# Kernel optimization log

Measured on AMD Instinct MI355X. Metric: run time of the kernel, lower is better.

Reference implementation:

```python
import jax, jax.numpy as jnp
import numpy as np

B, N = 8, 2048
IN_DIM, MEM_DIM, CTX_DIM = 256, 256, 128

def _linear_params(key, out_dim, in_dim):
    kw, kb = jax.random.split(key)
    bound = 1.0 / np.sqrt(in_dim)
    W = jax.random.uniform(kw, (out_dim, in_dim), jnp.float32, -bound, bound)
    b = jax.random.uniform(kb, (out_dim,), jnp.float32, -bound, bound)
    return W, b

def setup_inputs() -> dict:
    key = jax.random.key(0)
    ks = jax.random.split(key, 8)
    Wq, bq = _linear_params(ks[0], CTX_DIM, IN_DIM)
    Wk, bk = _linear_params(ks[1], CTX_DIM, MEM_DIM)
    Wv, bv = _linear_params(ks[2], MEM_DIM, MEM_DIM)
    Wu, bu = _linear_params(ks[3], MEM_DIM, IN_DIM + MEM_DIM)
    Wr, br = _linear_params(ks[4], MEM_DIM, IN_DIM + MEM_DIM)
    Wc, bc = _linear_params(ks[5], MEM_DIM, IN_DIM + MEM_DIM)
    input_tensor = jax.random.normal(ks[6], (B, N, IN_DIM), jnp.float32)
    previous_memory = jax.random.normal(ks[7], (B, N, MEM_DIM), jnp.float32)
    return dict(input_tensor=input_tensor, previous_memory=previous_memory,
                Wq=Wq, bq=bq, Wk=Wk, bk=bk, Wv=Wv, bv=bv,
                Wu=Wu, bu=bu, Wr=Wr, br=br, Wc=Wc, bc=bc)

def reference(input_tensor, previous_memory, Wq, bq, Wk, bk, Wv, bv, Wu, bu, Wr, br, Wc, bc):
    # QKV projections (torch Linear: y = x @ W.T + b)
    query = jnp.einsum('bnd,cd->bnc', input_tensor, Wq) + bq        # [B,N,CTX]
    key = jnp.einsum('bnm,cm->bnc', previous_memory, Wk) + bk       # [B,N,CTX]
    value = jnp.einsum('bnm,vm->bnv', previous_memory, Wv) + bv     # [B,N,MEM]
    attention_scores = jnp.einsum('bqc,bkc->bqk', query, key)        # [B,N,N]
    attention_probs = jax.nn.softmax(attention_scores, axis=-1)
    context_vector = jnp.einsum('bqk,bkv->bqv', attention_probs, value)  # computed but unused downstream, as in original
    combined = jnp.concatenate([input_tensor, previous_memory], axis=-1)  # [B,N,IN+MEM]
    update_gate = jax.nn.sigmoid(jnp.einsum('bnd,md->bnm', combined, Wu) + bu)
    reset_gate = jax.nn.sigmoid(jnp.einsum('bnd,md->bnm', combined, Wr) + br)
    cand_in = jnp.concatenate([input_tensor, reset_gate * previous_memory], axis=-1)
    candidate_memory = jnp.tanh(jnp.einsum('bnd,md->bnm', cand_in, Wc) + bc)
    new_memory = (1.0 - update_gate) * previous_memory + update_gate * candidate_memory
    return new_memory, attention_probs
```

## Files before the change

kernel.cpp:

```cpp
#include <hip/hip_runtime.h>


typedef _Float16 half8 __attribute__((ext_vector_type(8)));
typedef _Float16 half4 __attribute__((ext_vector_type(4)));
typedef float floatx4 __attribute__((ext_vector_type(4)));

#define MFMA16(a, b, c) __builtin_amdgcn_mfma_f32_16x16x32_f16((a), (b), (c), 0, 0, 0)

#define OFF_WQH 0
#define OFF_WQL 32768
#define OFF_WKH 65536
#define OFF_WKL 98304
#define OFF_WUH 131072
#define OFF_WRH 262144
#define OFF_WCH 393216
#define OFF_Q   524288
#define OFF_K   2621440

__device__ __forceinline__ void gload16(const void* g, void* l) {
  __builtin_amdgcn_global_load_lds((const __attribute__((address_space(1))) unsigned int*)g,
                                   (__attribute__((address_space(3))) unsigned int*)l, 16, 0, 0);
}

__global__ __launch_bounds__(256) void k0_convert(
    const float* __restrict__ Wq, const float* __restrict__ Wk,
    const float* __restrict__ Wu, const float* __restrict__ Wr,
    const float* __restrict__ Wc, _Float16* __restrict__ ws)
{
  int i = blockIdx.x * 256 + threadIdx.x;
  if (i < 32768) {
    float w = Wq[i];
    _Float16 h = (_Float16)w;
    ws[OFF_WQH + i] = h;
    ws[OFF_WQL + i] = (_Float16)(w - (float)h);
  } else if (i < 65536) {
    int j = i - 32768;
    float w = Wk[j];
    _Float16 h = (_Float16)w;
    ws[OFF_WKH + j] = h;
    ws[OFF_WKL + j] = (_Float16)(w - (float)h);
  } else {
    int j = i - 65536;
    if (j < 131072)      ws[OFF_WUH + j]            = (_Float16)Wu[j];
    else if (j < 262144) ws[OFF_WRH + (j - 131072)] = (_Float16)Wr[j - 131072];
    else                 ws[OFF_WCH + (j - 262144)] = (_Float16)Wc[j - 262144];
  }
}

__global__ __launch_bounds__(512) void k1_proj(
    const float* __restrict__ input, const float* __restrict__ prev,
    const float* __restrict__ bq, const float* __restrict__ bk,
    _Float16* __restrict__ ws)
{
  __shared__ char smem[2 * 8192];
  const int which = blockIdx.y;
  const float* x = which ? prev : input;
  const _Float16* WH = ws + (which ? OFF_WKH : OFF_WQH);
  const _Float16* WL = ws + (which ? OFF_WKL : OFF_WQL);
  const float* bias = which ? bk : bq;
  _Float16* out = ws + (which ? OFF_K : OFF_Q);

  const int tid = threadIdx.x, w = tid >> 6, l = tid & 63;
  const int lr = l & 15, lg = l >> 4;
  const int rows0 = blockIdx.x * 64;
  const int c = w * 16 + lr;

  half8 bh[8], blo[8];
#pragma unroll
  for (int ks = 0; ks < 8; ++ks) {
    bh[ks]  = *(const half8*)(WH + (size_t)c * 256 + ks * 32 + lg * 8);
    blo[ks] = *(const half8*)(WL + (size_t)c * 256 + ks * 32 + lg * 8);
  }
  const float bv = bias[c];

  const int srow = tid >> 5, scol = (tid & 31) * 8;
  const int ssz = (srow & 7) << 4;
  floatx4 st0, st1;

#define K1_LOAD(ch) { const float* src = x + ((size_t)rows0 + (ch) * 16 + srow) * 256 + scol; \
  st0 = *(const floatx4*)src; st1 = *(const floatx4*)(src + 4); }
#define K1_WRITE(ch) { char* bufw = smem + ((ch) & 1) * 8192; \
  half8 h; \
  _Pragma("unroll") for (int j = 0; j < 4; ++j) { \
    h[j] = (_Float16)st0[j]; h[4+j] = (_Float16)st1[j]; } \
  *(half8*)(bufw + srow * 512 + ((scol * 2) ^ ssz)) = h; }

  K1_LOAD(0); K1_WRITE(0);
  __syncthreads();
#pragma unroll 1
  for (int ch = 0; ch < 4; ++ch) {
    if (ch < 3) K1_LOAD(ch + 1);
    const char* buf = smem + (ch & 1) * 8192;
    floatx4 acc = {0.f, 0.f, 0.f, 0.f};
    const int base = lr * 512, sz = (lr & 7) << 4;
#pragma unroll
    for (int ks = 0; ks < 8; ++ks) {
      half8 ah = *(const half8*)(buf + base + ((ks * 64 + lg * 16) ^ sz));
      acc = MFMA16(ah, bh[ks], acc);
      acc = MFMA16(ah, blo[ks], acc);
    }
#pragma unroll
    for (int j = 0; j < 4; ++j)
      out[((size_t)rows0 + ch * 16 + lg * 4 + j) * 128 + c] = (_Float16)(acc[j] + bv);
    if (ch < 3) K1_WRITE(ch + 1);
    __syncthreads();
  }
}

__global__ __launch_bounds__(512) void k2ru(
    const float* __restrict__ input, const float* __restrict__ prev,
    const float* __restrict__ br, const float* __restrict__ bu,
    const _Float16* __restrict__ ws,
    _Float16* __restrict__ t_sc, _Float16* __restrict__ u_sc)
{
  __shared__ char smem[2 * 16384];
  const int tid = threadIdx.x, w = tid >> 6, l = tid & 63;
  const int lr = l & 15, lg = l >> 4;
  const int rows0 = blockIdx.x * 128;
  const int isU = w >> 2;
  const int c = blockIdx.y * 64 + (w & 3) * 16 + lr;

  const _Float16* W = ws + (isU ? OFF_WUH : OFF_WRH);
  half8 bw[16];
#pragma unroll
  for (int ks = 0; ks < 16; ++ks)
    bw[ks] = *(const half8*)(W + (size_t)c * 512 + ks * 32 + lg * 8);
  const float bv = (isU ? bu : br)[c];

  const int srow = tid >> 5, scol = (tid & 31) * 8;
  const int ssz = (srow & 7) << 4;
  floatx4 sI0, sI1, sP0, sP1;

#define K2RU_LOAD(ch) { \
  const float* si = input + ((size_t)rows0 + (ch) * 16 + srow) * 256 + scol; \
  const float* sp = prev  + ((size_t)rows0 + (ch) * 16 + srow) * 256 + scol; \
  sI0 = *(const floatx4*)si; sI1 = *(const floatx4*)(si + 4); \
  sP0 = *(const floatx4*)sp; sP1 = *(const floatx4*)(sp + 4); }
#define K2RU_WRITE(ch) { char* bufw = smem + ((ch) & 1) * 16384; \
  half8 hi, hp; \
  _Pragma("unroll") for (int j = 0; j < 4; ++j) { \
    hi[j] = (_Float16)sI0[j]; hi[4+j] = (_Float16)sI1[j]; \
    hp[j] = (_Float16)sP0[j]; hp[4+j] = (_Float16)sP1[j]; } \
  int o = srow * 1024 + ((scol * 2) ^ ssz); \
  *(half8*)(bufw + o) = hi; *(half8*)(bufw + o + 512) = hp; }

  K2RU_LOAD(0); K2RU_WRITE(0);
  __syncthreads();
#pragma unroll 1
  for (int ch = 0; ch < 8; ++ch) {
    if (ch < 7) K2RU_LOAD(ch + 1);
    const char* buf = smem + (ch & 1) * 16384;
    floatx4 acc = {0.f, 0.f, 0.f, 0.f};
    const int base = lr * 1024, sz = (lr & 7) << 4;
#pragma unroll
    for (int ks = 0; ks < 16; ++ks) {
      half8 a = *(const half8*)(buf + base + ((ks * 64 + lg * 16) ^ sz));
      acc = MFMA16(a, bw[ks], acc);
    }
#pragma unroll
    for (int j = 0; j < 4; ++j) {
      const int crow = lg * 4 + j;
      const size_t grow = (size_t)rows0 + ch * 16 + crow;
      float g = 1.f / (1.f + __expf(-(acc[j] + bv)));
      if (!isU) {
        float m = (float)*(const _Float16*)(buf + crow * 1024 + 512 + ((c * 2) ^ ((crow & 7) << 4)));
        t_sc[grow * 256 + c] = (_Float16)(g * m);
      } else {
        u_sc[grow * 256 + c] = (_Float16)g;
      }
    }
    if (ch < 7) K2RU_WRITE(ch + 1);
    __syncthreads();
  }
}

__global__ __launch_bounds__(512) void k2c(
    const float* __restrict__ input, const float* __restrict__ prev,
    const float* __restrict__ bc, const _Float16* __restrict__ ws,
    const _Float16* __restrict__ t_sc, const _Float16* __restrict__ u_sc,
    float* __restrict__ out0)
{
  __shared__ char smem[2 * 16384];
  const int tid = threadIdx.x, w = tid >> 6, l = tid & 63;
  const int lr = l & 15, lg = l >> 4;
  const int rows0 = blockIdx.x * 64;
  const int c = blockIdx.y * 128 + w * 16 + lr;

  half8 bw[16];
#pragma unroll
  for (int ks = 0; ks < 16; ++ks)
    bw[ks] = *(const half8*)(ws + OFF_WCH + (size_t)c * 512 + ks * 32 + lg * 8);
  const float bv = bc[c];

  const int srow = tid >> 5, scol = (tid & 31) * 8;
  const int ssz = (srow & 7) << 4;
  floatx4 sI0, sI1;
  half8 sT;

#define K2C_LOAD(ch) { \
  const float* si = input + ((size_t)rows0 + (ch) * 16 + srow) * 256 + scol; \
  sI0 = *(const floatx4*)si; sI1 = *(const floatx4*)(si + 4); \
  sT = *(const half8*)(t_sc + ((size_t)rows0 + (ch) * 16 + srow) * 256 + scol); }
#define K2C_WRITE(ch) { char* bufw = smem + ((ch) & 1) * 16384; \
  half8 hi; \
  _Pragma("unroll") for (int j = 0; j < 4; ++j) { hi[j] = (_Float16)sI0[j]; hi[4+j] = (_Float16)sI1[j]; } \
  int o = srow * 1024 + ((scol * 2) ^ ssz); \
  *(half8*)(bufw + o) = hi; *(half8*)(bufw + o + 512) = sT; }

  K2C_LOAD(0); K2C_WRITE(0);
  __syncthreads();
#pragma unroll 1
  for (int ch = 0; ch < 4; ++ch) {
    if (ch < 3) K2C_LOAD(ch + 1);
    const char* buf = smem + (ch & 1) * 16384;
    floatx4 acc = {0.f, 0.f, 0.f, 0.f};
    const int base = lr * 1024, sz = (lr & 7) << 4;
#pragma unroll
    for (int ks = 0; ks < 16; ++ks) {
      half8 a = *(const half8*)(buf + base + ((ks * 64 + lg * 16) ^ sz));
      acc = MFMA16(a, bw[ks], acc);
    }
#pragma unroll
    for (int j = 0; j < 4; ++j) {
      const size_t grow = (size_t)rows0 + ch * 16 + lg * 4 + j;
      float e2 = __expf(2.f * (acc[j] + bv));
      float cg = (e2 - 1.f) / (e2 + 1.f);
      float u = (float)u_sc[grow * 256 + c];
      float m = prev[grow * 256 + c];
      out0[grow * 256 + c] = (1.f - u) * m + u * cg;
    }
    if (ch < 3) K2C_WRITE(ch + 1);
    __syncthreads();
  }
}

#define K3_STAGE(Kg, dst, ch) { \
  const char* g_ = (Kg) + (ch) * 32768; \
  _Pragma("unroll") for (int i_ = 0; i_ < 4; ++i_) { \
    int o_ = w * 1024 + i_ * 8192 + l * 16; \
    int row_ = o_ >> 8, col_ = o_ & 255; \
    gload16(g_ + row_ * 256 + (col_ ^ ((row_ & 7) << 4)), (dst) + w * 1024 + i_ * 8192); } }

__global__ __launch_bounds__(512) void k3a_sums(
    const _Float16* __restrict__ ws, float* __restrict__ part)
{
  __shared__ char kbuf[2][32768];
  const int b = blockIdx.x, q0 = blockIdx.y * 128, kh = blockIdx.z;
  const int tid = threadIdx.x, w = tid >> 6, l = tid & 63;
  const int lr = l & 15, lg = l >> 4;

  const _Float16* Q = ws + OFF_Q + ((size_t)b * 2048 + q0 + w * 16) * 128;
  const char* Kg = (const char*)(ws + OFF_K + ((size_t)b * 2048 + kh * 512) * 128);

  half8 qf[4];
#pragma unroll
  for (int ks = 0; ks < 4; ++ks)
    qf[ks] = *(const half8*)(Q + (size_t)lr * 128 + ks * 32 + lg * 8);

  K3_STAGE(Kg, kbuf[0], 0);
  __syncthreads();

  float se = 0.f;
#pragma unroll 1
  for (int ch = 0; ch < 4; ++ch) {
    if (ch < 3) K3_STAGE(Kg, kbuf[(ch + 1) & 1], ch + 1);
    const char* buf = kbuf[ch & 1];
#pragma unroll
    for (int kt = 0; kt < 8; ++kt) {
      const int kk = kt * 16 + lr;
      const int kbase = kk * 256, ksz = (kk & 7) << 4;
      half8 kf[4];
#pragma unroll
      for (int ks = 0; ks < 4; ++ks)
        kf[ks] = *(const half8*)(buf + kbase + ((ks * 64 + lg * 16) ^ ksz));
      floatx4 acc = {0.f, 0.f, 0.f, 0.f};
#pragma unroll
      for (int ks = 0; ks < 4; ++ks) acc = MFMA16(kf[ks], qf[ks], acc);
#pragma unroll
      for (int j = 0; j < 4; ++j) se += __expf(acc[j] - 14.f);
    }
    __syncthreads();
  }
  se += __shfl_xor(se, 16);
  se += __shfl_xor(se, 32);
  if (lg == 0)
    part[((size_t)b * 4 + kh) * 2048 + q0 + w * 16 + lr] = se;
}

__global__ __launch_bounds__(512) void k3b_store(
    const _Float16* __restrict__ ws, const float* __restrict__ part,
    float* __restrict__ out1)
{
  __shared__ char kbuf[2][32768];
  const int b = blockIdx.x, q0 = blockIdx.y * 128, kh = blockIdx.z;
  const int tid = threadIdx.x, w = tid >> 6, l = tid & 63;
  const int lr = l & 15, lg = l >> 4;

  const int q = q0 + w * 16 + lr;
  const _Float16* Q = ws + OFF_Q + ((size_t)b * 2048 + q0 + w * 16) * 128;
  const char* Kg = (const char*)(ws + OFF_K + ((size_t)b * 2048 + kh * 512) * 128);

  half8 qf[4];
#pragma unroll
  for (int ks = 0; ks < 4; ++ks)
    qf[ks] = *(const half8*)(Q + (size_t)lr * 128 + ks * 32 + lg * 8);
  const float inv = 1.f / (part[(size_t)(b * 4 + 0) * 2048 + q] +
                           part[(size_t)(b * 4 + 1) * 2048 + q] +
                           part[(size_t)(b * 4 + 2) * 2048 + q] +
                           part[(size_t)(b * 4 + 3) * 2048 + q]);

  K3_STAGE(Kg, kbuf[0], 0);
  __syncthreads();

  float* orow = out1 + ((size_t)b * 2048 + q) * 2048 + kh * 512;
#pragma unroll 1
  for (int ch = 0; ch < 4; ++ch) {
    if (ch < 3) K3_STAGE(Kg, kbuf[(ch + 1) & 1], ch + 1);
    const char* buf = kbuf[ch & 1];
#pragma unroll
    for (int kt = 0; kt < 8; ++kt) {
      const int kk = kt * 16 + lr;
      const int kbase = kk * 256, ksz = (kk & 7) << 4;
      half8 kf[4];
#pragma unroll
      for (int ks = 0; ks < 4; ++ks)
        kf[ks] = *(const half8*)(buf + kbase + ((ks * 64 + lg * 16) ^ ksz));
      floatx4 acc = {0.f, 0.f, 0.f, 0.f};
#pragma unroll
      for (int ks = 0; ks < 4; ++ks) acc = MFMA16(kf[ks], qf[ks], acc);
      floatx4 v;
#pragma unroll
      for (int j = 0; j < 4; ++j) v[j] = __expf(acc[j] - 14.f) * inv;
      *(floatx4*)(orow + ch * 128 + kt * 16 + lg * 4) = v;
    }
    __syncthreads();
  }
}

extern "C" void kernel_launch(void* const* d_in, const int* in_sizes, int n_in,
                              void* d_out, int out_size, void* d_ws, size_t ws_size,
                              hipStream_t stream)
{
  const float* input = (const float*)d_in[0];
  const float* prev  = (const float*)d_in[1];
  const float* Wq = (const float*)d_in[2];
  const float* bq = (const float*)d_in[3];
  const float* Wk = (const float*)d_in[4];
  const float* bk = (const float*)d_in[5];
  const float* Wu = (const float*)d_in[8];
  const float* bu = (const float*)d_in[9];
  const float* Wr = (const float*)d_in[10];
  const float* br = (const float*)d_in[11];
  const float* Wc = (const float*)d_in[12];
  const float* bc = (const float*)d_in[13];

  float* out0 = (float*)d_out;
  float* out1 = out0 + (size_t)8 * 2048 * 256;
  _Float16* ws = (_Float16*)d_ws;

  _Float16* t_sc = (_Float16*)out1;
  _Float16* u_sc = (_Float16*)out1 + 4194304;
  float* part = (float*)ws;

  hipLaunchKernelGGL(k0_convert, dim3(1792), dim3(256), 0, stream, Wq, Wk, Wu, Wr, Wc, ws);
  hipLaunchKernelGGL(k1_proj,    dim3(256, 2), dim3(512), 0, stream, input, prev, bq, bk, ws);
  hipLaunchKernelGGL(k2ru,       dim3(128, 4), dim3(512), 0, stream, input, prev, br, bu, ws, t_sc, u_sc);
  hipLaunchKernelGGL(k2c,        dim3(256, 2), dim3(512), 0, stream, input, prev, bc, ws, t_sc, u_sc, out0);
  hipLaunchKernelGGL(k3a_sums,   dim3(8, 16, 4), dim3(512), 0, stream, ws, part);
  hipLaunchKernelGGL(k3b_store,  dim3(8, 16, 4), dim3(512), 0, stream, ws, part, out1);
}
```

Measured before the change: 109.5 us.

## Merge independent stages into two fused launches and convert weights inline

```diff
diff --git a/kernel.cpp b/kernel.cpp
--- a/kernel.cpp
+++ b/kernel.cpp
@@ -7,13 +7,6 @@
 
 #define MFMA16(a, b, c) __builtin_amdgcn_mfma_f32_16x16x32_f16((a), (b), (c), 0, 0, 0)
 
-#define OFF_WQH 0
-#define OFF_WQL 32768
-#define OFF_WKH 65536
-#define OFF_WKL 98304
-#define OFF_WUH 131072
-#define OFF_WRH 262144
-#define OFF_WCH 393216
 #define OFF_Q   524288
 #define OFF_K   2621440
 
@@ -22,114 +15,41 @@
                                    (__attribute__((address_space(3))) unsigned int*)l, 16, 0, 0);
 }
 
-__global__ __launch_bounds__(256) void k0_convert(
-    const float* __restrict__ Wq, const float* __restrict__ Wk,
-    const float* __restrict__ Wu, const float* __restrict__ Wr,
-    const float* __restrict__ Wc, _Float16* __restrict__ ws)
+__global__ __launch_bounds__(512, 4) void kA(
+    const float* __restrict__ input, const float* __restrict__ prev,
+    const float* __restrict__ Wq, const float* __restrict__ bq,
+    const float* __restrict__ Wk, const float* __restrict__ bk,
+    const float* __restrict__ Wr, const float* __restrict__ br,
+    const float* __restrict__ Wu, const float* __restrict__ bu,
+    _Float16* __restrict__ ws,
+    _Float16* __restrict__ t_sc, _Float16* __restrict__ u_sc)
 {
-  int i = blockIdx.x * 256 + threadIdx.x;
-  if (i < 32768) {
-    float w = Wq[i];
-    _Float16 h = (_Float16)w;
-    ws[OFF_WQH + i] = h;
-    ws[OFF_WQL + i] = (_Float16)(w - (float)h);
-  } else if (i < 65536) {
-    int j = i - 32768;
-    float w = Wk[j];
-    _Float16 h = (_Float16)w;
-    ws[OFF_WKH + j] = h;
-    ws[OFF_WKL + j] = (_Float16)(w - (float)h);
-  } else {
-    int j = i - 65536;
-    if (j < 131072)      ws[OFF_WUH + j]            = (_Float16)Wu[j];
-    else if (j < 262144) ws[OFF_WRH + (j - 131072)] = (_Float16)Wr[j - 131072];
-    else                 ws[OFF_WCH + (j - 262144)] = (_Float16)Wc[j - 262144];
-  }
-}
-
-__global__ __launch_bounds__(512) void k1_proj(
-    const float* __restrict__ input, const float* __restrict__ prev,
-    const float* __restrict__ bq, const float* __restrict__ bk,
-    _Float16* __restrict__ ws)
-{
-  __shared__ char smem[2 * 8192];
-  const int which = blockIdx.y;
-  const float* x = which ? prev : input;
-  const _Float16* WH = ws + (which ? OFF_WKH : OFF_WQH);
-  const _Float16* WL = ws + (which ? OFF_WKL : OFF_WQL);
-  const float* bias = which ? bk : bq;
-  _Float16* out = ws + (which ? OFF_K : OFF_Q);
-
+  __shared__ char smem[32768];
   const int tid = threadIdx.x, w = tid >> 6, l = tid & 63;
   const int lr = l & 15, lg = l >> 4;
-  const int rows0 = blockIdx.x * 64;
-  const int c = w * 16 + lr;
-
-  half8 bh[8], blo[8];
-#pragma unroll
-  for (int ks = 0; ks < 8; ++ks) {
-    bh[ks]  = *(const half8*)(WH + (size_t)c * 256 + ks * 32 + lg * 8);
-    blo[ks] = *(const half8*)(WL + (size_t)c * 256 + ks * 32 + lg * 8);
-  }
-  const float bv = bias[c];
-
-  const int srow = tid >> 5, scol = (tid & 31) * 8;
-  const int ssz = (srow & 7) << 4;
-  floatx4 st0, st1;
-
-#define K1_LOAD(ch) { const float* src = x + ((size_t)rows0 + (ch) * 16 + srow) * 256 + scol; \
-  st0 = *(const floatx4*)src; st1 = *(const floatx4*)(src + 4); }
-#define K1_WRITE(ch) { char* bufw = smem + ((ch) & 1) * 8192; \
-  half8 h; \
-  _Pragma("unroll") for (int j = 0; j < 4; ++j) { \
-    h[j] = (_Float16)st0[j]; h[4+j] = (_Float16)st1[j]; } \
-  *(half8*)(bufw + srow * 512 + ((scol * 2) ^ ssz)) = h; }
-
-  K1_LOAD(0); K1_WRITE(0);
-  __syncthreads();
-#pragma unroll 1
-  for (int ch = 0; ch < 4; ++ch) {
-    if (ch < 3) K1_LOAD(ch + 1);
-    const char* buf = smem + (ch & 1) * 8192;
-    floatx4 acc = {0.f, 0.f, 0.f, 0.f};
-    const int base = lr * 512, sz = (lr & 7) << 4;
-#pragma unroll
-    for (int ks = 0; ks < 8; ++ks) {
-      half8 ah = *(const half8*)(buf + base + ((ks * 64 + lg * 16) ^ sz));
-      acc = MFMA16(ah, bh[ks], acc);
-      acc = MFMA16(ah, blo[ks], acc);
-    }
-#pragma unroll
-    for (int j = 0; j < 4; ++j)
-      out[((size_t)rows0 + ch * 16 + lg * 4 + j) * 128 + c] = (_Float16)(acc[j] + bv);
-    if (ch < 3) K1_WRITE(ch + 1);
-    __syncthreads();
-  }
-}
-
-__global__ __launch_bounds__(512) void k2ru(
-    const float* __restrict__ input, const float* __restrict__ prev,
-    const float* __restrict__ br, const float* __restrict__ bu,
-    const _Float16* __restrict__ ws,
-    _Float16* __restrict__ t_sc, _Float16* __restrict__ u_sc)
-{
-  __shared__ char smem[2 * 16384];
-  const int tid = threadIdx.x, w = tid >> 6, l = tid & 63;
-  const int lr = l & 15, lg = l >> 4;
-  const int rows0 = blockIdx.x * 128;
-  const int isU = w >> 2;
-  const int c = blockIdx.y * 64 + (w & 3) * 16 + lr;
-
-  const _Float16* W = ws + (isU ? OFF_WUH : OFF_WRH);
-  half8 bw[16];
-#pragma unroll
-  for (int ks = 0; ks < 16; ++ks)
-    bw[ks] = *(const half8*)(W + (size_t)c * 512 + ks * 32 + lg * 8);
-  const float bv = (isU ? bu : br)[c];
-
-  const int srow = tid >> 5, scol = (tid & 31) * 8;
-  const int ssz = (srow & 7) << 4;
-  floatx4 sI0, sI1, sP0, sP1;
+
+  if (blockIdx.x < 512) {
+    const int b2 = blockIdx.x;
+    const int rows0 = (b2 & 127) * 128;
+    const int isU = w >> 2;
+    const int c = (b2 >> 7) * 64 + (w & 3) * 16 + lr;
+
+    const float* Wf = isU ? Wu : Wr;
+    half8 bw[16];
+#pragma unroll
+    for (int ks = 0; ks < 16; ++ks) {
+      floatx4 w0 = *(const floatx4*)(Wf + (size_t)c * 512 + ks * 32 + lg * 8);
+      floatx4 w1 = *(const floatx4*)(Wf + (size_t)c * 512 + ks * 32 + lg * 8 + 4);
+      half8 h;
+#pragma unroll
+      for (int j = 0; j < 4; ++j) { h[j] = (_Float16)w0[j]; h[4 + j] = (_Float16)w1[j]; }
+      bw[ks] = h;
+    }
+    const float bv = (isU ? bu : br)[c];
+
+    const int srow = tid >> 5, scol = (tid & 31) * 8;
+    const int ssz = (srow & 7) << 4;
+    floatx4 sI0, sI1, sP0, sP1;
 
 #define K2RU_LOAD(ch) { \
   const float* si = input + ((size_t)rows0 + (ch) * 16 + srow) * 256 + scol; \
@@ -144,58 +64,176 @@
   int o = srow * 1024 + ((scol * 2) ^ ssz); \
   *(half8*)(bufw + o) = hi; *(half8*)(bufw + o + 512) = hp; }
 
-  K2RU_LOAD(0); K2RU_WRITE(0);
-  __syncthreads();
-#pragma unroll 1
-  for (int ch = 0; ch < 8; ++ch) {
-    if (ch < 7) K2RU_LOAD(ch + 1);
-    const char* buf = smem + (ch & 1) * 16384;
-    floatx4 acc = {0.f, 0.f, 0.f, 0.f};
-    const int base = lr * 1024, sz = (lr & 7) << 4;
-#pragma unroll
-    for (int ks = 0; ks < 16; ++ks) {
-      half8 a = *(const half8*)(buf + base + ((ks * 64 + lg * 16) ^ sz));
-      acc = MFMA16(a, bw[ks], acc);
-    }
-#pragma unroll
-    for (int j = 0; j < 4; ++j) {
-      const int crow = lg * 4 + j;
-      const size_t grow = (size_t)rows0 + ch * 16 + crow;
-      float g = 1.f / (1.f + __expf(-(acc[j] + bv)));
-      if (!isU) {
-        float m = (float)*(const _Float16*)(buf + crow * 1024 + 512 + ((c * 2) ^ ((crow & 7) << 4)));
-        t_sc[grow * 256 + c] = (_Float16)(g * m);
-      } else {
-        u_sc[grow * 256 + c] = (_Float16)g;
-      }
-    }
-    if (ch < 7) K2RU_WRITE(ch + 1);
-    __syncthreads();
+    K2RU_LOAD(0); K2RU_WRITE(0);
+    __syncthreads();
+#pragma unroll 1
+    for (int ch = 0; ch < 8; ++ch) {
+      if (ch < 7) K2RU_LOAD(ch + 1);
+      const char* buf = smem + (ch & 1) * 16384;
+      floatx4 acc = {0.f, 0.f, 0.f, 0.f};
+      const int base = lr * 1024, sz = (lr & 7) << 4;
+#pragma unroll
+      for (int ks = 0; ks < 16; ++ks) {
+        half8 a = *(const half8*)(buf + base + ((ks * 64 + lg * 16) ^ sz));
+        acc = MFMA16(a, bw[ks], acc);
+      }
+#pragma unroll
+      for (int j = 0; j < 4; ++j) {
+        const int crow = lg * 4 + j;
+        const size_t grow = (size_t)rows0 + ch * 16 + crow;
+        float g = 1.f / (1.f + __expf(-(acc[j] + bv)));
+        if (!isU) {
+          float m = (float)*(const _Float16*)(buf + crow * 1024 + 512 + ((c * 2) ^ ((crow & 7) << 4)));
+          t_sc[grow * 256 + c] = (_Float16)(g * m);
+        } else {
+          u_sc[grow * 256 + c] = (_Float16)g;
+        }
+      }
+      if (ch < 7) K2RU_WRITE(ch + 1);
+      __syncthreads();
+    }
+  } else {
+    const int b1 = blockIdx.x - 512;
+    const int which = b1 >> 8;
+    const int rows0 = (b1 & 255) * 64;
+    const float* x = which ? prev : input;
+    const float* Wf = which ? Wk : Wq;
+    const float* bias = which ? bk : bq;
+    _Float16* out = ws + (which ? OFF_K : OFF_Q);
+    const int c = w * 16 + lr;
+
+    half8 bh[8], blo[8];
+#pragma unroll
+    for (int ks = 0; ks < 8; ++ks) {
+      floatx4 w0 = *(const floatx4*)(Wf + (size_t)c * 256 + ks * 32 + lg * 8);
+      floatx4 w1 = *(const floatx4*)(Wf + (size_t)c * 256 + ks * 32 + lg * 8 + 4);
+      half8 h, lo;
+#pragma unroll
+      for (int j = 0; j < 4; ++j) {
+        _Float16 h0 = (_Float16)w0[j];
+        h[j] = h0; lo[j] = (_Float16)(w0[j] - (float)h0);
+        _Float16 h1 = (_Float16)w1[j];
+        h[4 + j] = h1; lo[4 + j] = (_Float16)(w1[j] - (float)h1);
+      }
+      bh[ks] = h; blo[ks] = lo;
+    }
+    const float bv = bias[c];
+
+    const int srow = tid >> 5, scol = (tid & 31) * 8;
+    const int ssz = (srow & 7) << 4;
+    floatx4 st0, st1;
+
+#define K1_LOAD(ch) { const float* src = x + ((size_t)rows0 + (ch) * 16 + srow) * 256 + scol; \
+  st0 = *(const floatx4*)src; st1 = *(const floatx4*)(src + 4); }
+#define K1_WRITE(ch) { char* bufw = smem + ((ch) & 1) * 8192; \
+  half8 h; \
+  _Pragma("unroll") for (int j = 0; j < 4; ++j) { \
+    h[j] = (_Float16)st0[j]; h[4+j] = (_Float16)st1[j]; } \
+  *(half8*)(bufw + srow * 512 + ((scol * 2) ^ ssz)) = h; }
+
+    K1_LOAD(0); K1_WRITE(0);
+    __syncthreads();
+#pragma unroll 1
+    for (int ch = 0; ch < 4; ++ch) {
+      if (ch < 3) K1_LOAD(ch + 1);
+      const char* buf = smem + (ch & 1) * 8192;
+      floatx4 acc = {0.f, 0.f, 0.f, 0.f};
+      const int base = lr * 512, sz = (lr & 7) << 4;
+#pragma unroll
+      for (int ks = 0; ks < 8; ++ks) {
+        half8 ah = *(const half8*)(buf + base + ((ks * 64 + lg * 16) ^ sz));
+        acc = MFMA16(ah, bh[ks], acc);
+        acc = MFMA16(ah, blo[ks], acc);
+      }
+#pragma unroll
+      for (int j = 0; j < 4; ++j)
+        out[((size_t)rows0 + ch * 16 + lg * 4 + j) * 128 + c] = (_Float16)(acc[j] + bv);
+      if (ch < 3) K1_WRITE(ch + 1);
+      __syncthreads();
+    }
   }
 }
 
-__global__ __launch_bounds__(512) void k2c(
+#define K3_STAGE(Kg, dst, ch) { \
+  const char* g_ = (Kg) + (ch) * 32768; \
+  _Pragma("unroll") for (int i_ = 0; i_ < 4; ++i_) { \
+    int o_ = w * 1024 + i_ * 8192 + l * 16; \
+    int row_ = o_ >> 8, col_ = o_ & 255; \
+    gload16(g_ + row_ * 256 + (col_ ^ ((row_ & 7) << 4)), (dst) + w * 1024 + i_ * 8192); } }
+
+__global__ __launch_bounds__(512, 4) void kB(
     const float* __restrict__ input, const float* __restrict__ prev,
-    const float* __restrict__ bc, const _Float16* __restrict__ ws,
+    const float* __restrict__ Wc, const float* __restrict__ bc,
+    const _Float16* __restrict__ ws, float* __restrict__ part,
     const _Float16* __restrict__ t_sc, const _Float16* __restrict__ u_sc,
     float* __restrict__ out0)
 {
-  __shared__ char smem[2 * 16384];
+  __shared__ char smem[65536];
   const int tid = threadIdx.x, w = tid >> 6, l = tid & 63;
   const int lr = l & 15, lg = l >> 4;
-  const int rows0 = blockIdx.x * 64;
-  const int c = blockIdx.y * 128 + w * 16 + lr;
-
-  half8 bw[16];
-#pragma unroll
-  for (int ks = 0; ks < 16; ++ks)
-    bw[ks] = *(const half8*)(ws + OFF_WCH + (size_t)c * 512 + ks * 32 + lg * 8);
-  const float bv = bc[c];
-
-  const int srow = tid >> 5, scol = (tid & 31) * 8;
-  const int ssz = (srow & 7) << 4;
-  floatx4 sI0, sI1;
-  half8 sT;
+
+  if (blockIdx.x < 512) {
+    const int b3 = blockIdx.x;
+    const int b = b3 & 7, q0 = ((b3 >> 3) & 15) * 128, kh = b3 >> 7;
+
+    const _Float16* Q = ws + OFF_Q + ((size_t)b * 2048 + q0 + w * 16) * 128;
+    const char* Kg = (const char*)(ws + OFF_K + ((size_t)b * 2048 + kh * 512) * 128);
+
+    half8 qf[4];
+#pragma unroll
+    for (int ks = 0; ks < 4; ++ks)
+      qf[ks] = *(const half8*)(Q + (size_t)lr * 128 + ks * 32 + lg * 8);
+
+    char* kbuf0 = smem, * kbuf1 = smem + 32768;
+    K3_STAGE(Kg, kbuf0, 0);
+    __syncthreads();
+
+    float se = 0.f;
+#pragma unroll 1
+    for (int ch = 0; ch < 4; ++ch) {
+      if (ch < 3) K3_STAGE(Kg, ((ch + 1) & 1) ? kbuf1 : kbuf0, ch + 1);
+      const char* buf = (ch & 1) ? kbuf1 : kbuf0;
+#pragma unroll
+      for (int kt = 0; kt < 8; ++kt) {
+        const int kk = kt * 16 + lr;
+        const int kbase = kk * 256, ksz = (kk & 7) << 4;
+        half8 kf[4];
+#pragma unroll
+        for (int ks = 0; ks < 4; ++ks)
+          kf[ks] = *(const half8*)(buf + kbase + ((ks * 64 + lg * 16) ^ ksz));
+        floatx4 acc = {0.f, 0.f, 0.f, 0.f};
+#pragma unroll
+        for (int ks = 0; ks < 4; ++ks) acc = MFMA16(kf[ks], qf[ks], acc);
+#pragma unroll
+        for (int j = 0; j < 4; ++j) se += __expf(acc[j] - 14.f);
+      }
+      __syncthreads();
+    }
+    se += __shfl_xor(se, 16);
+    se += __shfl_xor(se, 32);
+    if (lg == 0)
+      part[((size_t)b * 4 + kh) * 2048 + q0 + w * 16 + lr] = se;
+  } else {
+    const int b2 = blockIdx.x - 512;
+    const int rows0 = (b2 & 255) * 64;
+    const int c = (b2 >> 8) * 128 + w * 16 + lr;
+
+    half8 bw[16];
+#pragma unroll
+    for (int ks = 0; ks < 16; ++ks) {
+      floatx4 w0 = *(const floatx4*)(Wc + (size_t)c * 512 + ks * 32 + lg * 8);
+      floatx4 w1 = *(const floatx4*)(Wc + (size_t)c * 512 + ks * 32 + lg * 8 + 4);
+      half8 h;
+#pragma unroll
+      for (int j = 0; j < 4; ++j) { h[j] = (_Float16)w0[j]; h[4 + j] = (_Float16)w1[j]; }
+      bw[ks] = h;
+    }
+    const float bv = bc[c];
+
+    const int srow = tid >> 5, scol = (tid & 31) * 8;
+    const int ssz = (srow & 7) << 4;
+    floatx4 sI0, sI1;
+    half8 sT;
 
 #define K2C_LOAD(ch) { \
   const float* si = input + ((size_t)rows0 + (ch) * 16 + srow) * 256 + scol; \
@@ -207,84 +245,32 @@
   int o = srow * 1024 + ((scol * 2) ^ ssz); \
   *(half8*)(bufw + o) = hi; *(half8*)(bufw + o + 512) = sT; }
 
-  K2C_LOAD(0); K2C_WRITE(0);
-  __syncthreads();
-#pragma unroll 1
-  for (int ch = 0; ch < 4; ++ch) {
-    if (ch < 3) K2C_LOAD(ch + 1);
-    const char* buf = smem + (ch & 1) * 16384;
-    floatx4 acc = {0.f, 0.f, 0.f, 0.f};
-    const int base = lr * 1024, sz = (lr & 7) << 4;
-#pragma unroll
-    for (int ks = 0; ks < 16; ++ks) {
-      half8 a = *(const half8*)(buf + base + ((ks * 64 + lg * 16) ^ sz));
-      acc = MFMA16(a, bw[ks], acc);
-    }
-#pragma unroll
-    for (int j = 0; j < 4; ++j) {
-      const size_t grow = (size_t)rows0 + ch * 16 + lg * 4 + j;
-      float e2 = __expf(2.f * (acc[j] + bv));
-      float cg = (e2 - 1.f) / (e2 + 1.f);
-      float u = (float)u_sc[grow * 256 + c];
-      float m = prev[grow * 256 + c];
-      out0[grow * 256 + c] = (1.f - u) * m + u * cg;
-    }
-    if (ch < 3) K2C_WRITE(ch + 1);
-    __syncthreads();
+    K2C_LOAD(0); K2C_WRITE(0);
+    __syncthreads();
+#pragma unroll 1
+    for (int ch = 0; ch < 4; ++ch) {
+      if (ch < 3) K2C_LOAD(ch + 1);
+      const char* buf = smem + (ch & 1) * 16384;
+      floatx4 acc = {0.f, 0.f, 0.f, 0.f};
+      const int base = lr * 1024, sz = (lr & 7) << 4;
+#pragma unroll
+      for (int ks = 0; ks < 16; ++ks) {
+        half8 a = *(const half8*)(buf + base + ((ks * 64 + lg * 16) ^ sz));
+        acc = MFMA16(a, bw[ks], acc);
+      }
+#pragma unroll
+      for (int j = 0; j < 4; ++j) {
+        const size_t grow = (size_t)rows0 + ch * 16 + lg * 4 + j;
+        float e2 = __expf(2.f * (acc[j] + bv));
+        float cg = (e2 - 1.f) / (e2 + 1.f);
+        float u = (float)u_sc[grow * 256 + c];
+        float m = prev[grow * 256 + c];
+        out0[grow * 256 + c] = (1.f - u) * m + u * cg;
+      }
+      if (ch < 3) K2C_WRITE(ch + 1);
+      __syncthreads();
+    }
   }
-}
-
-#define K3_STAGE(Kg, dst, ch) { \
-  const char* g_ = (Kg) + (ch) * 32768; \
-  _Pragma("unroll") for (int i_ = 0; i_ < 4; ++i_) { \
-    int o_ = w * 1024 + i_ * 8192 + l * 16; \
-    int row_ = o_ >> 8, col_ = o_ & 255; \
-    gload16(g_ + row_ * 256 + (col_ ^ ((row_ & 7) << 4)), (dst) + w * 1024 + i_ * 8192); } }
-
-__global__ __launch_bounds__(512) void k3a_sums(
-    const _Float16* __restrict__ ws, float* __restrict__ part)
-{
-  __shared__ char kbuf[2][32768];
-  const int b = blockIdx.x, q0 = blockIdx.y * 128, kh = blockIdx.z;
-  const int tid = threadIdx.x, w = tid >> 6, l = tid & 63;
-  const int lr = l & 15, lg = l >> 4;
-
-  const _Float16* Q = ws + OFF_Q + ((size_t)b * 2048 + q0 + w * 16) * 128;
-  const char* Kg = (const char*)(ws + OFF_K + ((size_t)b * 2048 + kh * 512) * 128);
-
-  half8 qf[4];
-#pragma unroll
-  for (int ks = 0; ks < 4; ++ks)
-    qf[ks] = *(const half8*)(Q + (size_t)lr * 128 + ks * 32 + lg * 8);
-
-  K3_STAGE(Kg, kbuf[0], 0);
-  __syncthreads();
-
-  float se = 0.f;
-#pragma unroll 1
-  for (int ch = 0; ch < 4; ++ch) {
-    if (ch < 3) K3_STAGE(Kg, kbuf[(ch + 1) & 1], ch + 1);
-    const char* buf = kbuf[ch & 1];
-#pragma unroll
-    for (int kt = 0; kt < 8; ++kt) {
-      const int kk = kt * 16 + lr;
-      const int kbase = kk * 256, ksz = (kk & 7) << 4;
-      half8 kf[4];
-#pragma unroll
-      for (int ks = 0; ks < 4; ++ks)
-        kf[ks] = *(const half8*)(buf + kbase + ((ks * 64 + lg * 16) ^ ksz));
-      floatx4 acc = {0.f, 0.f, 0.f, 0.f};
-#pragma unroll
-      for (int ks = 0; ks < 4; ++ks) acc = MFMA16(kf[ks], qf[ks], acc);
-#pragma unroll
-      for (int j = 0; j < 4; ++j) se += __expf(acc[j] - 14.f);
-    }
-    __syncthreads();
-  }
-  se += __shfl_xor(se, 16);
-  se += __shfl_xor(se, 32);
-  if (lg == 0)
-    part[((size_t)b * 4 + kh) * 2048 + q0 + w * 16 + lr] = se;
 }
 
 __global__ __launch_bounds__(512) void k3b_store(
@@ -362,10 +348,9 @@
   _Float16* u_sc = (_Float16*)out1 + 4194304;
   float* part = (float*)ws;
 
-  hipLaunchKernelGGL(k0_convert, dim3(1792), dim3(256), 0, stream, Wq, Wk, Wu, Wr, Wc, ws);
-  hipLaunchKernelGGL(k1_proj,    dim3(256, 2), dim3(512), 0, stream, input, prev, bq, bk, ws);
-  hipLaunchKernelGGL(k2ru,       dim3(128, 4), dim3(512), 0, stream, input, prev, br, bu, ws, t_sc, u_sc);
-  hipLaunchKernelGGL(k2c,        dim3(256, 2), dim3(512), 0, stream, input, prev, bc, ws, t_sc, u_sc, out0);
-  hipLaunchKernelGGL(k3a_sums,   dim3(8, 16, 4), dim3(512), 0, stream, ws, part);
-  hipLaunchKernelGGL(k3b_store,  dim3(8, 16, 4), dim3(512), 0, stream, ws, part, out1);
-}
+  hipLaunchKernelGGL(kA, dim3(1024), dim3(512), 0, stream,
+                     input, prev, Wq, bq, Wk, bk, Wr, br, Wu, bu, ws, t_sc, u_sc);
+  hipLaunchKernelGGL(kB, dim3(1024), dim3(512), 0, stream,
+                     input, prev, Wc, bc, ws, part, t_sc, u_sc, out0);
+  hipLaunchKernelGGL(k3b_store, dim3(8, 16, 4), dim3(512), 0, stream, ws, part, out1);
+}
```

New measurement: 110.3 us. No clear change (+0.8%).

## Fuse candidate-memory and softmax-store kernels into one horizontally fused launch

Applied to the files above, without the earlier changes.

```diff
diff --git a/kernel.cpp b/kernel.cpp
--- a/kernel.cpp
+++ b/kernel.cpp
@@ -2,7 +2,6 @@
 
 
 typedef _Float16 half8 __attribute__((ext_vector_type(8)));
-typedef _Float16 half4 __attribute__((ext_vector_type(4)));
 typedef float floatx4 __attribute__((ext_vector_type(4)));
 
 #define MFMA16(a, b, c) __builtin_amdgcn_mfma_f32_16x16x32_f16((a), (b), (c), 0, 0, 0)
@@ -16,6 +15,8 @@
 #define OFF_WCH 393216
 #define OFF_Q   524288
 #define OFF_K   2621440
+#define OFF_T   4718592
+#define OFF_U   8912896
 
 __device__ __forceinline__ void gload16(const void* g, void* l) {
   __builtin_amdgcn_global_load_lds((const __attribute__((address_space(1))) unsigned int*)g,
@@ -174,17 +175,34 @@
   }
 }
 
-__global__ __launch_bounds__(512) void k2c(
+#define K2C_LOAD(ch) { \
+  const float* si = input + ((size_t)rows0 + (ch) * 16 + srow) * 256 + scol; \
+  sI0 = *(const floatx4*)si; sI1 = *(const floatx4*)(si + 4); \
+  sT = *(const half8*)(t_sc + ((size_t)rows0 + (ch) * 16 + srow) * 256 + scol); }
+#define K2C_WRITE(ch) { char* bufw = smemc + ((ch) & 1) * 16384; \
+  half8 hi; \
+  _Pragma("unroll") for (int j = 0; j < 4; ++j) { hi[j] = (_Float16)sI0[j]; hi[4+j] = (_Float16)sI1[j]; } \
+  int o = srow * 1024 + ((scol * 2) ^ ssz); \
+  *(half8*)(bufw + o) = hi; *(half8*)(bufw + o + 512) = sT; }
+
+#define K3_STAGE(Kg, dst, ch) { \
+  const char* g_ = (Kg) + (ch) * 32768; \
+  _Pragma("unroll") for (int i_ = 0; i_ < 4; ++i_) { \
+    int o_ = w * 1024 + i_ * 8192 + l * 16; \
+    int row_ = o_ >> 8, col_ = o_ & 255; \
+    gload16(g_ + row_ * 256 + (col_ ^ ((row_ & 7) << 4)), (dst) + w * 1024 + i_ * 8192); } }
+
+__device__ __forceinline__ void k2c_body(
+    char* smemc, int job, int tid,
     const float* __restrict__ input, const float* __restrict__ prev,
     const float* __restrict__ bc, const _Float16* __restrict__ ws,
     const _Float16* __restrict__ t_sc, const _Float16* __restrict__ u_sc,
     float* __restrict__ out0)
 {
-  __shared__ char smem[2 * 16384];
-  const int tid = threadIdx.x, w = tid >> 6, l = tid & 63;
+  const int w = tid >> 6, l = tid & 63;
   const int lr = l & 15, lg = l >> 4;
-  const int rows0 = blockIdx.x * 64;
-  const int c = blockIdx.y * 128 + w * 16 + lr;
+  const int rows0 = (job & 255) * 64;
+  const int c = (job >> 8) * 128 + w * 16 + lr;
 
   half8 bw[16];
 #pragma unroll
@@ -196,23 +214,13 @@
   const int ssz = (srow & 7) << 4;
   floatx4 sI0, sI1;
   half8 sT;
-
-#define K2C_LOAD(ch) { \
-  const float* si = input + ((size_t)rows0 + (ch) * 16 + srow) * 256 + scol; \
-  sI0 = *(const floatx4*)si; sI1 = *(const floatx4*)(si + 4); \
-  sT = *(const half8*)(t_sc + ((size_t)rows0 + (ch) * 16 + srow) * 256 + scol); }
-#define K2C_WRITE(ch) { char* bufw = smem + ((ch) & 1) * 16384; \
-  half8 hi; \
-  _Pragma("unroll") for (int j = 0; j < 4; ++j) { hi[j] = (_Float16)sI0[j]; hi[4+j] = (_Float16)sI1[j]; } \
-  int o = srow * 1024 + ((scol * 2) ^ ssz); \
-  *(half8*)(bufw + o) = hi; *(half8*)(bufw + o + 512) = sT; }
 
   K2C_LOAD(0); K2C_WRITE(0);
   __syncthreads();
 #pragma unroll 1
   for (int ch = 0; ch < 4; ++ch) {
     if (ch < 3) K2C_LOAD(ch + 1);
-    const char* buf = smem + (ch & 1) * 16384;
+    const char* buf = smemc + (ch & 1) * 16384;
     floatx4 acc = {0.f, 0.f, 0.f, 0.f};
     const int base = lr * 1024, sz = (lr & 7) << 4;
 #pragma unroll
@@ -234,67 +242,14 @@
   }
 }
 
-#define K3_STAGE(Kg, dst, ch) { \
-  const char* g_ = (Kg) + (ch) * 32768; \
-  _Pragma("unroll") for (int i_ = 0; i_ < 4; ++i_) { \
-    int o_ = w * 1024 + i_ * 8192 + l * 16; \
-    int row_ = o_ >> 8, col_ = o_ & 255; \
-    gload16(g_ + row_ * 256 + (col_ ^ ((row_ & 7) << 4)), (dst) + w * 1024 + i_ * 8192); } }
-
-__global__ __launch_bounds__(512) void k3a_sums(
-    const _Float16* __restrict__ ws, float* __restrict__ part)
-{
-  __shared__ char kbuf[2][32768];
-  const int b = blockIdx.x, q0 = blockIdx.y * 128, kh = blockIdx.z;
-  const int tid = threadIdx.x, w = tid >> 6, l = tid & 63;
-  const int lr = l & 15, lg = l >> 4;
-
-  const _Float16* Q = ws + OFF_Q + ((size_t)b * 2048 + q0 + w * 16) * 128;
-  const char* Kg = (const char*)(ws + OFF_K + ((size_t)b * 2048 + kh * 512) * 128);
-
-  half8 qf[4];
-#pragma unroll
-  for (int ks = 0; ks < 4; ++ks)
-    qf[ks] = *(const half8*)(Q + (size_t)lr * 128 + ks * 32 + lg * 8);
-
-  K3_STAGE(Kg, kbuf[0], 0);
-  __syncthreads();
-
-  float se = 0.f;
-#pragma unroll 1
-  for (int ch = 0; ch < 4; ++ch) {
-    if (ch < 3) K3_STAGE(Kg, kbuf[(ch + 1) & 1], ch + 1);
-    const char* buf = kbuf[ch & 1];
-#pragma unroll
-    for (int kt = 0; kt < 8; ++kt) {
-      const int kk = kt * 16 + lr;
-      const int kbase = kk * 256, ksz = (kk & 7) << 4;
-      half8 kf[4];
-#pragma unroll
-      for (int ks = 0; ks < 4; ++ks)
-        kf[ks] = *(const half8*)(buf + kbase + ((ks * 64 + lg * 16) ^ ksz));
-      floatx4 acc = {0.f, 0.f, 0.f, 0.f};
-#pragma unroll
-      for (int ks = 0; ks < 4; ++ks) acc = MFMA16(kf[ks], qf[ks], acc);
-#pragma unroll
-      for (int j = 0; j < 4; ++j) se += __expf(acc[j] - 14.f);
-    }
-    __syncthreads();
-  }
-  se += __shfl_xor(se, 16);
-  se += __shfl_xor(se, 32);
-  if (lg == 0)
-    part[((size_t)b * 4 + kh) * 2048 + q0 + w * 16 + lr] = se;
-}
-
-__global__ __launch_bounds__(512) void k3b_store(
+__device__ __forceinline__ void k3b_body(
+    char* smem, int job, int tid,
     const _Float16* __restrict__ ws, const float* __restrict__ part,
     float* __restrict__ out1)
 {
-  __shared__ char kbuf[2][32768];
-  const int b = blockIdx.x, q0 = blockIdx.y * 128, kh = blockIdx.z;
-  const int tid = threadIdx.x, w = tid >> 6, l = tid & 63;
+  const int w = tid >> 6, l = tid & 63;
   const int lr = l & 15, lg = l >> 4;
+  const int b = job & 7, q0 = ((job >> 3) & 15) * 128, kh = job >> 7;
 
   const int q = q0 + w * 16 + lr;
   const _Float16* Q = ws + OFF_Q + ((size_t)b * 2048 + q0 + w * 16) * 128;
@@ -309,10 +264,55 @@
                            part[(size_t)(b * 4 + 2) * 2048 + q] +
                            part[(size_t)(b * 4 + 3) * 2048 + q]);
 
+  char* kbuf0 = smem; char* kbuf1 = smem + 32768;
+  K3_STAGE(Kg, kbuf0, 0);
+  __syncthreads();
+
+  float* orow = out1 + ((size_t)b * 2048 + q) * 2048 + kh * 512;
+#pragma unroll 1
+  for (int ch = 0; ch < 4; ++ch) {
+    if (ch < 3) K3_STAGE(Kg, ((ch + 1) & 1) ? kbuf1 : kbuf0, ch + 1);
+    const char* buf = (ch & 1) ? kbuf1 : kbuf0;
+#pragma unroll
+    for (int kt = 0; kt < 8; ++kt) {
+      const int kk = kt * 16 + lr;
+      const int kbase = kk * 256, ksz = (kk & 7) << 4;
+      half8 kf[4];
+#pragma unroll
+      for (int ks = 0; ks < 4; ++ks)
+        kf[ks] = *(const half8*)(buf + kbase + ((ks * 64 + lg * 16) ^ ksz));
+      floatx4 acc = {0.f, 0.f, 0.f, 0.f};
+#pragma unroll
+      for (int ks = 0; ks < 4; ++ks) acc = MFMA16(kf[ks], qf[ks], acc);
+      floatx4 v;
+#pragma unroll
+      for (int j = 0; j < 4; ++j) v[j] = __expf(acc[j] - 14.f) * inv;
+      *(floatx4*)(orow + ch * 128 + kt * 16 + lg * 4) = v;
+    }
+    __syncthreads();
+  }
+}
+
+__global__ __launch_bounds__(512) void k3a_sums(
+    const _Float16* __restrict__ ws, float* __restrict__ part)
+{
+  __shared__ char kbuf[2][32768];
+  const int b = blockIdx.x, q0 = blockIdx.y * 128, kh = blockIdx.z;
+  const int tid = threadIdx.x, w = tid >> 6, l = tid & 63;
+  const int lr = l & 15, lg = l >> 4;
+
+  const _Float16* Q = ws + OFF_Q + ((size_t)b * 2048 + q0 + w * 16) * 128;
+  const char* Kg = (const char*)(ws + OFF_K + ((size_t)b * 2048 + kh * 512) * 128);
+
+  half8 qf[4];
+#pragma unroll
+  for (int ks = 0; ks < 4; ++ks)
+    qf[ks] = *(const half8*)(Q + (size_t)lr * 128 + ks * 32 + lg * 8);
+
   K3_STAGE(Kg, kbuf[0], 0);
   __syncthreads();
 
-  float* orow = out1 + ((size_t)b * 2048 + q) * 2048 + kh * 512;
+  float se = 0.f;
 #pragma unroll 1
   for (int ch = 0; ch < 4; ++ch) {
     if (ch < 3) K3_STAGE(Kg, kbuf[(ch + 1) & 1], ch + 1);
@@ -328,13 +328,47 @@
       floatx4 acc = {0.f, 0.f, 0.f, 0.f};
 #pragma unroll
       for (int ks = 0; ks < 4; ++ks) acc = MFMA16(kf[ks], qf[ks], acc);
-      floatx4 v;
-#pragma unroll
-      for (int j = 0; j < 4; ++j) v[j] = __expf(acc[j] - 14.f) * inv;
-      *(floatx4*)(orow + ch * 128 + kt * 16 + lg * 4) = v;
+#pragma unroll
+      for (int j = 0; j < 4; ++j) se += __expf(acc[j] - 14.f);
     }
     __syncthreads();
   }
+  se += __shfl_xor(se, 16);
+  se += __shfl_xor(se, 32);
+  if (lg == 0)
+    part[((size_t)b * 4 + kh) * 2048 + q0 + w * 16 + lr] = se;
+}
+
+__global__ __launch_bounds__(512) void k2c_kernel(
+    const float* __restrict__ input, const float* __restrict__ prev,
+    const float* __restrict__ bc, const _Float16* __restrict__ ws,
+    const _Float16* __restrict__ t_sc, const _Float16* __restrict__ u_sc,
+    float* __restrict__ out0)
+{
+  __shared__ char smemc[2 * 16384];
+  k2c_body(smemc, blockIdx.x, threadIdx.x, input, prev, bc, ws, t_sc, u_sc, out0);
+}
+
+__global__ __launch_bounds__(512) void k3b_kernel(
+    const _Float16* __restrict__ ws, const float* __restrict__ part,
+    float* __restrict__ out1)
+{
+  __shared__ char smem[65536];
+  k3b_body(smem, blockIdx.x, threadIdx.x, ws, part, out1);
+}
+
+__global__ __launch_bounds__(512, 4) void kD(
+    const float* __restrict__ input, const float* __restrict__ prev,
+    const float* __restrict__ bc, const _Float16* __restrict__ ws,
+    const float* __restrict__ part,
+    const _Float16* __restrict__ t_sc, const _Float16* __restrict__ u_sc,
+    float* __restrict__ out0, float* __restrict__ out1)
+{
+  __shared__ char smem[65536];
+  if (blockIdx.x < 512)
+    k3b_body(smem, blockIdx.x, threadIdx.x, ws, part, out1);
+  else
+    k2c_body(smem, blockIdx.x - 512, threadIdx.x, input, prev, bc, ws, t_sc, u_sc, out0);
 }
 
 extern "C" void kernel_launch(void* const* d_in, const int* in_sizes, int n_in,
@@ -358,14 +392,25 @@
   float* out1 = out0 + (size_t)8 * 2048 * 256;
   _Float16* ws = (_Float16*)d_ws;
 
-  _Float16* t_sc = (_Float16*)out1;
-  _Float16* u_sc = (_Float16*)out1 + 4194304;
   float* part = (float*)ws;
+  const bool big = ws_size >= (size_t)26214400;
 
   hipLaunchKernelGGL(k0_convert, dim3(1792), dim3(256), 0, stream, Wq, Wk, Wu, Wr, Wc, ws);
   hipLaunchKernelGGL(k1_proj,    dim3(256, 2), dim3(512), 0, stream, input, prev, bq, bk, ws);
-  hipLaunchKernelGGL(k2ru,       dim3(128, 4), dim3(512), 0, stream, input, prev, br, bu, ws, t_sc, u_sc);
-  hipLaunchKernelGGL(k2c,        dim3(256, 2), dim3(512), 0, stream, input, prev, bc, ws, t_sc, u_sc, out0);
-  hipLaunchKernelGGL(k3a_sums,   dim3(8, 16, 4), dim3(512), 0, stream, ws, part);
-  hipLaunchKernelGGL(k3b_store,  dim3(8, 16, 4), dim3(512), 0, stream, ws, part, out1);
-}
+
+  if (big) {
+    _Float16* t_sc = ws + OFF_T;
+    _Float16* u_sc = ws + OFF_U;
+    hipLaunchKernelGGL(k2ru,     dim3(128, 4), dim3(512), 0, stream, input, prev, br, bu, ws, t_sc, u_sc);
+    hipLaunchKernelGGL(k3a_sums, dim3(8, 16, 4), dim3(512), 0, stream, ws, part);
+    hipLaunchKernelGGL(kD,       dim3(1024), dim3(512), 0, stream,
+                       input, prev, bc, ws, part, t_sc, u_sc, out0, out1);
+  } else {
+    _Float16* t_sc = (_Float16*)out1;
+    _Float16* u_sc = (_Float16*)out1 + 4194304;
+    hipLaunchKernelGGL(k2ru,       dim3(128, 4), dim3(512), 0, stream, input, prev, br, bu, ws, t_sc, u_sc);
+    hipLaunchKernelGGL(k2c_kernel, dim3(512), dim3(512), 0, stream, input, prev, bc, ws, t_sc, u_sc, out0);
+    hipLaunchKernelGGL(k3a_sums,   dim3(8, 16, 4), dim3(512), 0, stream, ws, part);
+    hipLaunchKernelGGL(k3b_kernel, dim3(512), dim3(512), 0, stream, ws, part, out1);
+  }
+}
```

Measured after the change: 105.7 us, median of 2. 3.5% less time.
